# Kernel tuning notes

Hardware: AMD Instinct MI355X
Metric: run time of the kernel (lower is better)

Reference implementation:

```python
import jax, jax.numpy as jnp
import numpy as np


def setup_inputs() -> dict:
    key = jax.random.key(0)
    k1, k2, k3 = jax.random.split(key, 3)
    B, T, D = 16, 2048, 256
    input_feature = jax.random.normal(k1, (B, T, 2 * D), dtype=jnp.float32)
    W = jax.random.normal(k2, (D, D), dtype=jnp.float32) * 0.05
    b = jax.random.normal(k3, (D,), dtype=jnp.float32) * 0.05
    return {"input_feature": input_feature, "W": W, "b": b}


def reference(input_feature, W, b):
    # chunk into two halves along last dim and sum -> h: [B, T, 256]
    h1, h2 = jnp.split(input_feature, 2, axis=-1)
    h = h1 + h2
    # attention_layer: Linear(256,256) + ReLU  (torch Linear: x @ W.T + b)
    atten_w = jax.nn.relu(jnp.einsum('btd,ed->bte', h, W) + b)  # [B, T, 256]
    m = jnp.tanh(h)
    # bmm(m, atten_w^T): scores [B, T, T]
    atten_context = jnp.einsum('btd,bsd->bts', m, atten_w)
    softmax_w = jax.nn.softmax(atten_context, axis=-1)
    # bmm(h^T, softmax_w): [B, 256, T]
    context = jnp.einsum('btd,bts->bds', h, softmax_w)
    # residual add with h^T
    return jnp.swapaxes(h, 1, 2) + context
```

## Files before the change

kernel.cpp:

```cpp
#include <hip/hip_runtime.h>
#include <hip/hip_bf16.h>
#include <math.h>


#define NB 16
#define NT 2048
#define ND 256

typedef __attribute__((ext_vector_type(4))) float f32x4;
typedef __attribute__((ext_vector_type(8))) short s16x8;
typedef __attribute__((ext_vector_type(4))) short s16x4;
typedef __attribute__((ext_vector_type(8))) _Float16 f16x8;
typedef unsigned short u16;

__device__ __forceinline__ u16 f2h(float x) {
  union { _Float16 h; u16 u; } v; v.h = (_Float16)x; return v.u;
}
__device__ __forceinline__ float h2f(u16 u) {
  union { u16 u; _Float16 h; } v; v.u = u; return (float)v.h;
}
__device__ __forceinline__ float tanh_fast(float x) {
  return 1.f - 2.f / (1.f + __expf(2.f * x));
}

__global__ __launch_bounds__(256, 8) void kA(const float* __restrict__ inF,
    u16* __restrict__ h16, u16* __restrict__ m16, u16* __restrict__ hfrag)
{
  __shared__ __attribute__((aligned(16))) u16 hld[32][264];
  const int blk = blockIdx.x;
  const int b   = blk >> 6;
  const int t0  = (blk & 63) << 5;
  const int tid = threadIdx.x;
  const int w    = tid >> 6;
  const int lane = tid & 63;
  const int rh   = lane >> 5;
  const int dseg = (lane & 31) << 3;
  #pragma unroll
  for (int it = 0; it < 4; ++it) {
    const int rloc = w * 8 + it * 2 + rh;
    const size_t grow = (size_t)(b * NT + t0 + rloc);
    const float* base = inF + grow * (2 * ND) + dseg;
    float4 a0 = *(const float4*)(base);
    float4 a1 = *(const float4*)(base + 4);
    float4 c0 = *(const float4*)(base + ND);
    float4 c1 = *(const float4*)(base + ND + 4);
    float hv[8] = {a0.x + c0.x, a0.y + c0.y, a0.z + c0.z, a0.w + c0.w,
                   a1.x + c1.x, a1.y + c1.y, a1.z + c1.z, a1.w + c1.w};
    s16x8 vh, vm;
    #pragma unroll
    for (int r = 0; r < 8; ++r) {
      vh[r] = (short)f2h(hv[r]);
      vm[r] = (short)f2h(tanh_fast(hv[r]));
    }
    *(s16x8*)&hld[rloc][dseg] = vh;
    __builtin_nontemporal_store(vh, (s16x8*)(h16 + grow * ND + dseg));
    __builtin_nontemporal_store(vm, (s16x8*)(m16 + grow * ND + dseg));
  }
  __syncthreads();
  u16* Hb = hfrag + (size_t)b * ND * NT;
  const int ti = t0 >> 5;
  #pragma unroll
  for (int s = 0; s < 4; ++s) {
    const int slot  = tid * 4 + s;
    const int dtile = slot >> 6;
    const int lp    = slot & 63;
    const int d  = dtile * 16 + (lp & 15);
    const int tb = (lp >> 4) * 8;
    s16x8 v;
    #pragma unroll
    for (int j = 0; j < 8; ++j) v[j] = (short)hld[tb + j][d];
    __builtin_nontemporal_store(v,
        (s16x8*)(Hb + (((size_t)dtile * (NT / 32) + ti) * 64 + lp) * 8));
  }
}

__global__ __launch_bounds__(256, 2) void kB(const u16* __restrict__ h16,
    const float* __restrict__ W, const float* __restrict__ bias, u16* __restrict__ aw16)
{
  __shared__ __attribute__((aligned(16))) u16 Wl[128][264];
  const int r0 = blockIdx.x << 7;
  const int e0 = blockIdx.y << 7;
  const int tid = threadIdx.x;
  #pragma unroll
  for (int rep = 0; rep < 16; ++rep) {
    const int idx = rep * 2048 + tid * 8;
    const int er = idx >> 8, col = idx & 255;
    float4 x0 = *(const float4*)(W + (size_t)(e0 + er) * ND + col);
    float4 x1 = *(const float4*)(W + (size_t)(e0 + er) * ND + col + 4);
    s16x8 v;
    v[0] = (short)f2h(x0.x); v[1] = (short)f2h(x0.y); v[2] = (short)f2h(x0.z); v[3] = (short)f2h(x0.w);
    v[4] = (short)f2h(x1.x); v[5] = (short)f2h(x1.y); v[6] = (short)f2h(x1.z); v[7] = (short)f2h(x1.w);
    *(s16x8*)&Wl[er][col] = v;
  }
  const int lane = tid & 63;
  const int w    = tid >> 6;
  const int l15  = lane & 15, kg = lane >> 4;
  float bv[8];
  #pragma unroll
  for (int et = 0; et < 8; ++et) bv[et] = bias[e0 + et * 16 + l15];
  f32x4 acc[2][8];
  #pragma unroll
  for (int rt = 0; rt < 2; ++rt)
    #pragma unroll
    for (int et = 0; et < 8; ++et) acc[rt][et] = (f32x4){0.f, 0.f, 0.f, 0.f};
  __syncthreads();
  #pragma unroll
  for (int ks = 0; ks < 8; ++ks) {
    f16x8 af[2];
    #pragma unroll
    for (int rt = 0; rt < 2; ++rt)
      af[rt] = *(const f16x8*)(h16 + (size_t)(r0 + w * 32 + rt * 16 + l15) * ND + ks * 32 + kg * 8);
    #pragma unroll
    for (int et = 0; et < 8; ++et) {
      f16x8 bf = *(const f16x8*)&Wl[et * 16 + l15][ks * 32 + kg * 8];
      #pragma unroll
      for (int rt = 0; rt < 2; ++rt)
        acc[rt][et] = __builtin_amdgcn_mfma_f32_16x16x32_f16(af[rt], bf, acc[rt][et], 0, 0, 0);
    }
  }
  __syncthreads();
  u16 (*awt)[132] = (u16 (*)[132])(&Wl[0][0]);
  #pragma unroll
  for (int rt = 0; rt < 2; ++rt)
    #pragma unroll
    for (int et = 0; et < 8; ++et) {
      const int e_loc = et * 16 + l15;
      #pragma unroll
      for (int r = 0; r < 4; ++r) {
        const int row_loc = w * 32 + rt * 16 + kg * 4 + r;
        float v = acc[rt][et][r] + bv[et];
        awt[row_loc][e_loc] = f2h(v > 0.f ? v : 0.f);
      }
    }
  __syncthreads();
  #pragma unroll
  for (int it = 0; it < 8; ++it) {
    const int rloc = it * 16 + w * 4 + (lane >> 4);
    const int sb   = (lane & 15) << 3;
    s16x8 v = *(const s16x8*)&awt[rloc][sb];
    __builtin_nontemporal_store(v, (s16x8*)(aw16 + (size_t)(r0 + rloc) * ND + e0 + sb));
  }
}

__global__ __launch_bounds__(512, 4) void k2z(
    const u16* __restrict__ m16, const u16* __restrict__ aw16,
    u16* __restrict__ Sfrag, float* __restrict__ Zarr)
{
  __shared__ __attribute__((aligned(16))) u16 awch[2][64][264];
  __shared__ float zp[2][64];
  const int tt  = blockIdx.x;
  const int b   = blockIdx.y;
  const int t0  = tt << 6;
  const int tid = threadIdx.x;
  const int lane = tid & 63;
  const int w    = tid >> 6;
  const int grp  = w >> 2;
  const int wl   = w & 3;
  const int l15 = lane & 15, kg = lane >> 4;
  f16x8 afr[8];
  const size_t abase = ((size_t)(b * NT + t0 + wl * 16 + l15)) * ND + kg * 8;
  #pragma unroll
  for (int ks = 0; ks < 8; ++ks) afr[ks] = *(const f16x8*)(m16 + abase + ks * 32);
  const u16* awb = aw16 + (size_t)b * NT * ND;
  u16* STb = Sfrag + (size_t)b * NT * NT;
  const int ti    = tt * 2 + (wl >> 1);
  const int lanep = l15 + 16 * ((wl & 1) * 2 + (kg >> 1));
  const int jp    = (kg & 1) * 4;
  auto stage = [&](int step, int buf) {
    const int s0 = step << 6;
    #pragma unroll
    for (int rep = 0; rep < 4; ++rep) {
      const int idx = rep * 4096 + tid * 8;
      const int srow = idx >> 8, col = idx & 255;
      *(s16x8*)&awch[buf][srow][col] = *(const s16x8*)(awb + (size_t)(s0 + srow) * ND + col);
    }
  };
  stage(0, 0);
  float zacc[4] = {0.f, 0.f, 0.f, 0.f};
  __syncthreads();
  for (int step = 0; step < 32; ++step) {
    const int c = step & 1;
    if (step < 31) stage(step + 1, c ^ 1);
    f32x4 accS[2];
    accS[0] = (f32x4){0.f, 0.f, 0.f, 0.f};
    accS[1] = (f32x4){0.f, 0.f, 0.f, 0.f};
    #pragma unroll
    for (int ks = 0; ks < 8; ++ks) {
      #pragma unroll
      for (int st = 0; st < 2; ++st) {
        f16x8 bf = *(const f16x8*)&awch[c][grp * 32 + st * 16 + l15][ks * 32 + kg * 8];
        accS[st] = __builtin_amdgcn_mfma_f32_16x16x32_f16(afr[ks], bf, accS[st], 0, 0, 0);
      }
    }
    #pragma unroll
    for (int st = 0; st < 2; ++st) {
      const int si = step * 4 + grp * 2 + st;
      s16x4 sv;
      #pragma unroll
      for (int r = 0; r < 4; ++r) sv[r] = (short)f2h(accS[st][r]);
      __builtin_nontemporal_store(sv,
          (s16x4*)(STb + (((size_t)si * 64 + ti) * 64 + lanep) * 8 + jp));
      #pragma unroll
      for (int r = 0; r < 4; ++r) zacc[r] += __expf(accS[st][r]);
    }
    __syncthreads();
  }
  #pragma unroll
  for (int r = 0; r < 4; ++r) {
    #pragma unroll
    for (int o = 1; o < 16; o <<= 1) zacc[r] += __shfl_xor(zacc[r], o, 64);
  }
  if (l15 == 0) {
    #pragma unroll
    for (int r = 0; r < 4; ++r) zp[grp][wl * 16 + kg * 4 + r] = zacc[r];
  }
  __syncthreads();
  if (tid < 64)
    Zarr[(size_t)b * NT + t0 + tid] = zp[0][tid] + zp[1][tid];
}

__global__ __launch_bounds__(512, 4) void k3o(
    const u16* __restrict__ Sfrag, const u16* __restrict__ hfrag,
    const float* __restrict__ Zarr, float* __restrict__ outp)
{
  __shared__ __attribute__((aligned(16))) u16 Pbuf[2][4][2][64][8];
  __shared__ float zld[NT];
  const int b   = blockIdx.y;
  const int s0t = blockIdx.x;
  const int tid = threadIdx.x;
  const int lane = tid & 63;
  const int w    = tid >> 6;
  const int l15 = lane & 15, kg = lane >> 4;
  const u16* Sb = Sfrag + (size_t)b * NT * NT;
  const u16* Hb = hfrag + (size_t)b * ND * NT;
  {
    float4 z = *(const float4*)(Zarr + (size_t)b * NT + tid * 4);
    zld[tid * 4 + 0] = 1.f / z.x;
    zld[tid * 4 + 1] = 1.f / z.y;
    zld[tid * 4 + 2] = 1.f / z.z;
    zld[tid * 4 + 3] = 1.f / z.w;
  }
  const int mst = w >> 1, mks = w & 1;
  const u16* sp = Sb + ((((size_t)(s0t * 4 + mst)) * 64 + mks) * 64 + lane) * 8;
  auto loadS = [&](int ch) -> s16x8 {
    return __builtin_nontemporal_load((const s16x8*)(sp + (size_t)ch * 1024));
  };
  auto expP = [&](s16x8 v, int ch) -> s16x8 {
    const float* rzp = &zld[(ch * 2 + mks) * 32 + kg * 8];
    float4 ra = *(const float4*)rzp;
    float4 rb = *(const float4*)(rzp + 4);
    const float rv[8] = {ra.x, ra.y, ra.z, ra.w, rb.x, rb.y, rb.z, rb.w};
    s16x8 p;
    #pragma unroll
    for (int j = 0; j < 8; ++j) p[j] = (short)f2h(__expf(h2f((u16)v[j])) * rv[j]);
    return p;
  };

  f32x4 acc[4][2];
  #pragma unroll
  for (int st = 0; st < 4; ++st) {
    acc[st][0] = (f32x4){0.f, 0.f, 0.f, 0.f};
    acc[st][1] = (f32x4){0.f, 0.f, 0.f, 0.f};
  }

  s16x8 d0 = loadS(0);
  s16x8 d1 = loadS(1);
  s16x8 d2 = loadS(2);
  __syncthreads();
  {
    s16x8 pr = expP(d0, 0);
    *(s16x8*)&Pbuf[0][mst][mks][lane][0] = pr;
  }
  __syncthreads();

  for (int ch = 0; ch < 32; ++ch) {
    const int cur = ch & 1;
    s16x8 prn;
    if (ch < 31) prn = expP(d1, ch + 1);
    d1 = d2;
    if (ch + 3 < 32) d2 = loadS(ch + 3);
    #pragma unroll
    for (int ks = 0; ks < 2; ++ks) {
      f16x8 pa[4];
      #pragma unroll
      for (int st = 0; st < 4; ++st)
        pa[st] = *(const f16x8*)&Pbuf[cur][st][ks][lane][0];
      #pragma unroll
      for (int dt = 0; dt < 2; ++dt) {
        f16x8 hb = *(const f16x8*)(Hb + (((size_t)(w * 2 + dt) * 64 + ch * 2 + ks) * 64 + lane) * 8);
        #pragma unroll
        for (int st = 0; st < 4; ++st)
          acc[st][dt] = __builtin_amdgcn_mfma_f32_16x16x32_f16(pa[st], hb, acc[st][dt], 0, 0, 0);
      }
    }
    if (ch < 31) *(s16x8*)&Pbuf[cur ^ 1][mst][mks][lane][0] = prn;
    __syncthreads();
  }
  #pragma unroll
  for (int st = 0; st < 4; ++st) {
    const int sb = s0t * 64 + st * 16 + kg * 4;
    #pragma unroll
    for (int dt = 0; dt < 2; ++dt) {
      const int d = w * 32 + dt * 16 + l15;
      const u16* hres = Hb + (((size_t)(w * 2 + dt) * 64 + (s0t * 2 + (st >> 1))) * 64
                        + (l15 + 16 * ((st & 1) * 2 + (kg >> 1)))) * 8 + (kg & 1) * 4;
      float4 o;
      o.x = acc[st][dt][0] + h2f(hres[0]);
      o.y = acc[st][dt][1] + h2f(hres[1]);
      o.z = acc[st][dt][2] + h2f(hres[2]);
      o.w = acc[st][dt][3] + h2f(hres[3]);
      *(float4*)(outp + ((size_t)(b * ND + d)) * NT + sb) = o;
    }
  }
}

extern "C" void kernel_launch(void* const* d_in, const int* in_sizes, int n_in,
                              void* d_out, int out_size, void* d_ws, size_t ws_size,
                              hipStream_t stream) {
  const float* inF  = (const float*)d_in[0];
  const float* W    = (const float*)d_in[1];
  const float* bias = (const float*)d_in[2];
  float* outp = (float*)d_out;

  const size_t SZ = (size_t)NB * NT * ND;
  u16* m16   = (u16*)d_ws;
  u16* hfrag = m16 + SZ;
  u16* aw16  = hfrag + SZ;
  float* Zarr = (float*)(aw16 + SZ);
  u16* Sfrag = (u16*)(Zarr + (size_t)NB * NT);
  u16* h16   = Sfrag;
  const size_t need = 3 * SZ * sizeof(u16) + (size_t)NB * NT * sizeof(float)
                    + (size_t)NB * NT * NT * sizeof(u16);
  if (ws_size < need) return;

  kA <<<dim3(NB * NT / 32), dim3(256), 0, stream>>>(inF, h16, m16, hfrag);
  kB <<<dim3(256, 2), dim3(256), 0, stream>>>(h16, W, bias, aw16);
  k2z<<<dim3(32, NB), dim3(512), 0, stream>>>(m16, aw16, Sfrag, Zarr);
  k3o<<<dim3(NT / 64, NB), dim3(512), 0, stream>>>(Sfrag, hfrag, Zarr, outp);
}
```

Baseline: 172.8 us.

## Halve k2z staging tile for occupancy and prefetch H fragments in k3o

The score kernel k2z now stages 32 rows of attention weights per step instead of 64 and runs twice as many steps. This halves its shared memory use and each wave's accumulators, and launch bounds are raised to allow 8 blocks per CU. The output kernel k3o unrolls its chunk loop by two and double-buffers the H fragments in registers, so global loads of H for the next chunk overlap the MFMAs of the current one. The cost is more barriers in k2z and higher register pressure in k3o.

```diff
diff --git a/kernel.cpp b/kernel.cpp
--- a/kernel.cpp
+++ b/kernel.cpp
@@ -142,11 +142,11 @@
   }
 }
 
-__global__ __launch_bounds__(512, 4) void k2z(
+__global__ __launch_bounds__(512, 8) void k2z(
     const u16* __restrict__ m16, const u16* __restrict__ aw16,
     u16* __restrict__ Sfrag, float* __restrict__ Zarr)
 {
-  __shared__ __attribute__((aligned(16))) u16 awch[2][64][264];
+  __shared__ __attribute__((aligned(16))) u16 awch[2][32][264];
   __shared__ float zp[2][64];
   const int tt  = blockIdx.x;
   const int b   = blockIdx.y;
@@ -167,9 +167,9 @@
   const int lanep = l15 + 16 * ((wl & 1) * 2 + (kg >> 1));
   const int jp    = (kg & 1) * 4;
   auto stage = [&](int step, int buf) {
-    const int s0 = step << 6;
-    #pragma unroll
-    for (int rep = 0; rep < 4; ++rep) {
+    const int s0 = step << 5;
+    #pragma unroll
+    for (int rep = 0; rep < 2; ++rep) {
       const int idx = rep * 4096 + tid * 8;
       const int srow = idx >> 8, col = idx & 255;
       *(s16x8*)&awch[buf][srow][col] = *(const s16x8*)(awb + (size_t)(s0 + srow) * ND + col);
@@ -178,31 +178,23 @@
   stage(0, 0);
   float zacc[4] = {0.f, 0.f, 0.f, 0.f};
   __syncthreads();
-  for (int step = 0; step < 32; ++step) {
+  for (int step = 0; step < 64; ++step) {
     const int c = step & 1;
-    if (step < 31) stage(step + 1, c ^ 1);
-    f32x4 accS[2];
-    accS[0] = (f32x4){0.f, 0.f, 0.f, 0.f};
-    accS[1] = (f32x4){0.f, 0.f, 0.f, 0.f};
+    if (step < 63) stage(step + 1, c ^ 1);
+    f32x4 accS = (f32x4){0.f, 0.f, 0.f, 0.f};
     #pragma unroll
     for (int ks = 0; ks < 8; ++ks) {
-      #pragma unroll
-      for (int st = 0; st < 2; ++st) {
-        f16x8 bf = *(const f16x8*)&awch[c][grp * 32 + st * 16 + l15][ks * 32 + kg * 8];
-        accS[st] = __builtin_amdgcn_mfma_f32_16x16x32_f16(afr[ks], bf, accS[st], 0, 0, 0);
-      }
-    }
-    #pragma unroll
-    for (int st = 0; st < 2; ++st) {
-      const int si = step * 4 + grp * 2 + st;
-      s16x4 sv;
-      #pragma unroll
-      for (int r = 0; r < 4; ++r) sv[r] = (short)f2h(accS[st][r]);
-      __builtin_nontemporal_store(sv,
-          (s16x4*)(STb + (((size_t)si * 64 + ti) * 64 + lanep) * 8 + jp));
-      #pragma unroll
-      for (int r = 0; r < 4; ++r) zacc[r] += __expf(accS[st][r]);
-    }
+      f16x8 bf = *(const f16x8*)&awch[c][grp * 16 + l15][ks * 32 + kg * 8];
+      accS = __builtin_amdgcn_mfma_f32_16x16x32_f16(afr[ks], bf, accS, 0, 0, 0);
+    }
+    const int si = step * 2 + grp;
+    s16x4 sv;
+    #pragma unroll
+    for (int r = 0; r < 4; ++r) sv[r] = (short)f2h(accS[r]);
+    __builtin_nontemporal_store(sv,
+        (s16x4*)(STb + (((size_t)si * 64 + ti) * 64 + lanep) * 8 + jp));
+    #pragma unroll
+    for (int r = 0; r < 4; ++r) zacc[r] += __expf(accS[r]);
     __syncthreads();
   }
   #pragma unroll
@@ -255,6 +247,13 @@
     for (int j = 0; j < 8; ++j) p[j] = (short)f2h(__expf(h2f((u16)v[j])) * rv[j]);
     return p;
   };
+  auto loadH = [&](f16x8 (&dst)[2][2], int ch) {
+    #pragma unroll
+    for (int dt = 0; dt < 2; ++dt)
+      #pragma unroll
+      for (int ks = 0; ks < 2; ++ks)
+        dst[dt][ks] = *(const f16x8*)(Hb + (((size_t)(w * 2 + dt) * 64 + ch * 2 + ks) * 64 + lane) * 8);
+  };
 
   f32x4 acc[4][2];
   #pragma unroll
@@ -262,10 +261,26 @@
     acc[st][0] = (f32x4){0.f, 0.f, 0.f, 0.f};
     acc[st][1] = (f32x4){0.f, 0.f, 0.f, 0.f};
   }
+  auto mfmaStep = [&](int cur, f16x8 (&hb)[2][2]) {
+    #pragma unroll
+    for (int ks = 0; ks < 2; ++ks) {
+      f16x8 pa[4];
+      #pragma unroll
+      for (int st = 0; st < 4; ++st)
+        pa[st] = *(const f16x8*)&Pbuf[cur][st][ks][lane][0];
+      #pragma unroll
+      for (int dt = 0; dt < 2; ++dt)
+        #pragma unroll
+        for (int st = 0; st < 4; ++st)
+          acc[st][dt] = __builtin_amdgcn_mfma_f32_16x16x32_f16(pa[st], hb[dt][ks], acc[st][dt], 0, 0, 0);
+    }
+  };
 
   s16x8 d0 = loadS(0);
   s16x8 d1 = loadS(1);
   s16x8 d2 = loadS(2);
+  f16x8 hA[2][2], hB[2][2];
+  loadH(hA, 0);
   __syncthreads();
   {
     s16x8 pr = expP(d0, 0);
@@ -273,27 +288,24 @@
   }
   __syncthreads();
 
-  for (int ch = 0; ch < 32; ++ch) {
-    const int cur = ch & 1;
-    s16x8 prn;
-    if (ch < 31) prn = expP(d1, ch + 1);
+  for (int ch = 0; ch < 32; ch += 2) {
+    loadH(hB, ch + 1);
+    {
+      s16x8 prn = expP(d1, ch + 1);
+      d1 = d2;
+      if (ch + 3 < 32) d2 = loadS(ch + 3);
+      mfmaStep(0, hA);
+      *(s16x8*)&Pbuf[1][mst][mks][lane][0] = prn;
+    }
+    __syncthreads();
+    if (ch + 2 < 32) loadH(hA, ch + 2);
+    const bool wr = (ch + 2 < 32);
+    s16x8 prn2;
+    if (wr) prn2 = expP(d1, ch + 2);
     d1 = d2;
-    if (ch + 3 < 32) d2 = loadS(ch + 3);
-    #pragma unroll
-    for (int ks = 0; ks < 2; ++ks) {
-      f16x8 pa[4];
-      #pragma unroll
-      for (int st = 0; st < 4; ++st)
-        pa[st] = *(const f16x8*)&Pbuf[cur][st][ks][lane][0];
-      #pragma unroll
-      for (int dt = 0; dt < 2; ++dt) {
-        f16x8 hb = *(const f16x8*)(Hb + (((size_t)(w * 2 + dt) * 64 + ch * 2 + ks) * 64 + lane) * 8);
-        #pragma unroll
-        for (int st = 0; st < 4; ++st)
-          acc[st][dt] = __builtin_amdgcn_mfma_f32_16x16x32_f16(pa[st], hb, acc[st][dt], 0, 0, 0);
-      }
-    }
-    if (ch < 31) *(s16x8*)&Pbuf[cur ^ 1][mst][mks][lane][0] = prn;
+    if (ch + 4 < 32) d2 = loadS(ch + 4);
+    mfmaStep(1, hB);
+    if (wr) *(s16x8*)&Pbuf[0][mst][mks][lane][0] = prn2;
     __syncthreads();
   }
   #pragma unroll
```

Result: slower. 218.4 us (+26.3%).

## Retile score and output GEMM wave mappings and use lightweight LDS barriers

Applied to the files above, without the earlier changes.

Replaces __syncthreads with a custom barrier that waits only on LDS/scalar counters, so outstanding global loads and stores are not drained at each barrier. Remaps waves in the score kernel so each wave reuses one LDS B-fragment across two A row-tiles. The partial Z sums are now reduced over four slots. In the output kernel each wave now computes 2 s-tiles by 4 d-tiles instead of 4 by 2, with H fragments prefetched at the top of each chunk. These changes cut LDS reads and barrier stalls, at the cost of more registers for the held fragments.

```diff
diff --git a/kernel.cpp b/kernel.cpp
--- a/kernel.cpp
+++ b/kernel.cpp
@@ -21,6 +21,12 @@
 }
 __device__ __forceinline__ float tanh_fast(float x) {
   return 1.f - 2.f / (1.f + __expf(2.f * x));
+}
+__device__ __forceinline__ void ldsbar() {
+  __builtin_amdgcn_sched_barrier(0);
+  asm volatile("s_waitcnt lgkmcnt(0)" ::: "memory");
+  __builtin_amdgcn_s_barrier();
+  __builtin_amdgcn_sched_barrier(0);
 }
 
 __global__ __launch_bounds__(256, 8) void kA(const float* __restrict__ inF,
@@ -56,7 +62,7 @@
     __builtin_nontemporal_store(vh, (s16x8*)(h16 + grow * ND + dseg));
     __builtin_nontemporal_store(vm, (s16x8*)(m16 + grow * ND + dseg));
   }
-  __syncthreads();
+  ldsbar();
   u16* Hb = hfrag + (size_t)b * ND * NT;
   const int ti = t0 >> 5;
   #pragma unroll
@@ -103,7 +109,7 @@
   for (int rt = 0; rt < 2; ++rt)
     #pragma unroll
     for (int et = 0; et < 8; ++et) acc[rt][et] = (f32x4){0.f, 0.f, 0.f, 0.f};
-  __syncthreads();
+  ldsbar();
   #pragma unroll
   for (int ks = 0; ks < 8; ++ks) {
     f16x8 af[2];
@@ -118,7 +124,7 @@
         acc[rt][et] = __builtin_amdgcn_mfma_f32_16x16x32_f16(af[rt], bf, acc[rt][et], 0, 0, 0);
     }
   }
-  __syncthreads();
+  ldsbar();
   u16 (*awt)[132] = (u16 (*)[132])(&Wl[0][0]);
   #pragma unroll
   for (int rt = 0; rt < 2; ++rt)
@@ -132,7 +138,7 @@
         awt[row_loc][e_loc] = f2h(v > 0.f ? v : 0.f);
       }
     }
-  __syncthreads();
+  ldsbar();
   #pragma unroll
   for (int it = 0; it < 8; ++it) {
     const int rloc = it * 16 + w * 4 + (lane >> 4);
@@ -147,37 +153,38 @@
     u16* __restrict__ Sfrag, float* __restrict__ Zarr)
 {
   __shared__ __attribute__((aligned(16))) u16 awch[2][64][264];
-  __shared__ float zp[2][64];
+  __shared__ float zp[4][64];
   const int tt  = blockIdx.x;
   const int b   = blockIdx.y;
   const int t0  = tt << 6;
   const int tid = threadIdx.x;
   const int lane = tid & 63;
   const int w    = tid >> 6;
-  const int grp  = w >> 2;
-  const int wl   = w & 3;
+  const int u    = w >> 2;
+  const int v    = w & 3;
   const int l15 = lane & 15, kg = lane >> 4;
-  f16x8 afr[8];
-  const size_t abase = ((size_t)(b * NT + t0 + wl * 16 + l15)) * ND + kg * 8;
-  #pragma unroll
-  for (int ks = 0; ks < 8; ++ks) afr[ks] = *(const f16x8*)(m16 + abase + ks * 32);
+  f16x8 afr2[2][8];
+  #pragma unroll
+  for (int i = 0; i < 2; ++i) {
+    const size_t ab = ((size_t)(b * NT + t0 + (u * 2 + i) * 16 + l15)) * ND + kg * 8;
+    #pragma unroll
+    for (int ks = 0; ks < 8; ++ks) afr2[i][ks] = *(const f16x8*)(m16 + ab + ks * 32);
+  }
   const u16* awb = aw16 + (size_t)b * NT * ND;
   u16* STb = Sfrag + (size_t)b * NT * NT;
-  const int ti    = tt * 2 + (wl >> 1);
-  const int lanep = l15 + 16 * ((wl & 1) * 2 + (kg >> 1));
-  const int jp    = (kg & 1) * 4;
+  const int ti = tt * 2 + u;
   auto stage = [&](int step, int buf) {
     const int s0 = step << 6;
     #pragma unroll
     for (int rep = 0; rep < 4; ++rep) {
       const int idx = rep * 4096 + tid * 8;
-      const int srow = idx >> 8, col = idx & 255;
-      *(s16x8*)&awch[buf][srow][col] = *(const s16x8*)(awb + (size_t)(s0 + srow) * ND + col);
+      *(s16x8*)&awch[buf][idx >> 8][idx & 255] =
+          *(const s16x8*)(awb + (size_t)(s0 + (idx >> 8)) * ND + (idx & 255));
     }
   };
   stage(0, 0);
-  float zacc[4] = {0.f, 0.f, 0.f, 0.f};
-  __syncthreads();
+  float zacc[2][4] = {{0.f,0.f,0.f,0.f},{0.f,0.f,0.f,0.f}};
+  ldsbar();
   for (int step = 0; step < 32; ++step) {
     const int c = step & 1;
     if (step < 31) stage(step + 1, c ^ 1);
@@ -186,37 +193,42 @@
     accS[1] = (f32x4){0.f, 0.f, 0.f, 0.f};
     #pragma unroll
     for (int ks = 0; ks < 8; ++ks) {
-      #pragma unroll
-      for (int st = 0; st < 2; ++st) {
-        f16x8 bf = *(const f16x8*)&awch[c][grp * 32 + st * 16 + l15][ks * 32 + kg * 8];
-        accS[st] = __builtin_amdgcn_mfma_f32_16x16x32_f16(afr[ks], bf, accS[st], 0, 0, 0);
-      }
-    }
-    #pragma unroll
-    for (int st = 0; st < 2; ++st) {
-      const int si = step * 4 + grp * 2 + st;
+      f16x8 bf = *(const f16x8*)&awch[c][v * 16 + l15][ks * 32 + kg * 8];
+      accS[0] = __builtin_amdgcn_mfma_f32_16x16x32_f16(afr2[0][ks], bf, accS[0], 0, 0, 0);
+      accS[1] = __builtin_amdgcn_mfma_f32_16x16x32_f16(afr2[1][ks], bf, accS[1], 0, 0, 0);
+    }
+    const int si = step * 4 + v;
+    #pragma unroll
+    for (int i = 0; i < 2; ++i) {
+      const int lanep = l15 + 16 * (i * 2 + (kg >> 1));
+      const int jp    = (kg & 1) * 4;
       s16x4 sv;
       #pragma unroll
-      for (int r = 0; r < 4; ++r) sv[r] = (short)f2h(accS[st][r]);
+      for (int r = 0; r < 4; ++r) sv[r] = (short)f2h(accS[i][r]);
       __builtin_nontemporal_store(sv,
           (s16x4*)(STb + (((size_t)si * 64 + ti) * 64 + lanep) * 8 + jp));
       #pragma unroll
-      for (int r = 0; r < 4; ++r) zacc[r] += __expf(accS[st][r]);
-    }
-    __syncthreads();
-  }
-  #pragma unroll
-  for (int r = 0; r < 4; ++r) {
-    #pragma unroll
-    for (int o = 1; o < 16; o <<= 1) zacc[r] += __shfl_xor(zacc[r], o, 64);
-  }
+      for (int r = 0; r < 4; ++r) zacc[i][r] += __expf(accS[i][r]);
+    }
+    ldsbar();
+  }
+  #pragma unroll
+  for (int i = 0; i < 2; ++i)
+    #pragma unroll
+    for (int r = 0; r < 4; ++r) {
+      #pragma unroll
+      for (int o = 1; o < 16; o <<= 1) zacc[i][r] += __shfl_xor(zacc[i][r], o, 64);
+    }
   if (l15 == 0) {
     #pragma unroll
-    for (int r = 0; r < 4; ++r) zp[grp][wl * 16 + kg * 4 + r] = zacc[r];
-  }
-  __syncthreads();
+    for (int i = 0; i < 2; ++i)
+      #pragma unroll
+      for (int r = 0; r < 4; ++r)
+        zp[v][(u * 2 + i) * 16 + kg * 4 + r] = zacc[i][r];
+  }
+  ldsbar();
   if (tid < 64)
-    Zarr[(size_t)b * NT + t0 + tid] = zp[0][tid] + zp[1][tid];
+    Zarr[(size_t)b * NT + t0 + tid] = zp[0][tid] + zp[1][tid] + zp[2][tid] + zp[3][tid];
 }
 
 __global__ __launch_bounds__(512, 4) void k3o(
@@ -230,6 +242,8 @@
   const int tid = threadIdx.x;
   const int lane = tid & 63;
   const int w    = tid >> 6;
+  const int sh   = w >> 2;
+  const int dq   = w & 3;
   const int l15 = lane & 15, kg = lane >> 4;
   const u16* Sb = Sfrag + (size_t)b * NT * NT;
   const u16* Hb = hfrag + (size_t)b * ND * NT;
@@ -256,54 +270,59 @@
     return p;
   };
 
-  f32x4 acc[4][2];
-  #pragma unroll
-  for (int st = 0; st < 4; ++st) {
-    acc[st][0] = (f32x4){0.f, 0.f, 0.f, 0.f};
-    acc[st][1] = (f32x4){0.f, 0.f, 0.f, 0.f};
-  }
+  f32x4 acc[2][4];
+  #pragma unroll
+  for (int st = 0; st < 2; ++st)
+    #pragma unroll
+    for (int dt = 0; dt < 4; ++dt) acc[st][dt] = (f32x4){0.f, 0.f, 0.f, 0.f};
 
   s16x8 d0 = loadS(0);
   s16x8 d1 = loadS(1);
   s16x8 d2 = loadS(2);
-  __syncthreads();
+  ldsbar();
   {
     s16x8 pr = expP(d0, 0);
     *(s16x8*)&Pbuf[0][mst][mks][lane][0] = pr;
   }
-  __syncthreads();
+  ldsbar();
 
   for (int ch = 0; ch < 32; ++ch) {
     const int cur = ch & 1;
+    f16x8 hb[4][2];
+    #pragma unroll
+    for (int dt = 0; dt < 4; ++dt)
+      #pragma unroll
+      for (int ks = 0; ks < 2; ++ks)
+        hb[dt][ks] = *(const f16x8*)(Hb + (((size_t)(dq * 4 + dt) * 64 + ch * 2 + ks) * 64 + lane) * 8);
     s16x8 prn;
     if (ch < 31) prn = expP(d1, ch + 1);
     d1 = d2;
     if (ch + 3 < 32) d2 = loadS(ch + 3);
     #pragma unroll
     for (int ks = 0; ks < 2; ++ks) {
-      f16x8 pa[4];
-      #pragma unroll
-      for (int st = 0; st < 4; ++st)
-        pa[st] = *(const f16x8*)&Pbuf[cur][st][ks][lane][0];
-      #pragma unroll
-      for (int dt = 0; dt < 2; ++dt) {
-        f16x8 hb = *(const f16x8*)(Hb + (((size_t)(w * 2 + dt) * 64 + ch * 2 + ks) * 64 + lane) * 8);
+      f16x8 pa[2];
+      #pragma unroll
+      for (int st = 0; st < 2; ++st)
+        pa[st] = *(const f16x8*)&Pbuf[cur][sh * 2 + st][ks][lane][0];
+      #pragma unroll
+      for (int dt = 0; dt < 4; ++dt)
         #pragma unroll
-        for (int st = 0; st < 4; ++st)
-          acc[st][dt] = __builtin_amdgcn_mfma_f32_16x16x32_f16(pa[st], hb, acc[st][dt], 0, 0, 0);
-      }
+        for (int st = 0; st < 2; ++st)
+          acc[st][dt] = __builtin_amdgcn_mfma_f32_16x16x32_f16(pa[st], hb[dt][ks], acc[st][dt], 0, 0, 0);
     }
     if (ch < 31) *(s16x8*)&Pbuf[cur ^ 1][mst][mks][lane][0] = prn;
-    __syncthreads();
-  }
-  #pragma unroll
-  for (int st = 0; st < 4; ++st) {
-    const int sb = s0t * 64 + st * 16 + kg * 4;
-    #pragma unroll
-    for (int dt = 0; dt < 2; ++dt) {
-      const int d = w * 32 + dt * 16 + l15;
-      const u16* hres = Hb + (((size_t)(w * 2 + dt) * 64 + (s0t * 2 + (st >> 1))) * 64
-                        + (l15 + 16 * ((st & 1) * 2 + (kg >> 1)))) * 8 + (kg & 1) * 4;
+    ldsbar();
+  }
+  #pragma unroll
+  for (int st = 0; st < 2; ++st) {
+    const int sg = sh * 2 + st;
+    const int sb = s0t * 64 + sg * 16 + kg * 4;
+    #pragma unroll
+    for (int dt = 0; dt < 4; ++dt) {
+      const int dd = dq * 4 + dt;
+      const int d  = dd * 16 + l15;
+      const u16* hres = Hb + (((size_t)dd * 64 + (s0t * 2 + (sg >> 1))) * 64
+                        + (l15 + 16 * ((sg & 1) * 2 + (kg >> 1)))) * 8 + (kg & 1) * 4;
       float4 o;
       o.x = acc[st][dt][0] + h2f(hres[0]);
       o.y = acc[st][dt][1] + h2f(hres[1]);
```

Measured after the change: 196.0 us. +13.4%, slower.
